# Performance work log

Measured on AMD Instinct MI355X. Metric: run time of the kernel, lower is better.

The kernel has to match this reference:

```python
import jax, jax.numpy as jnp
import numpy as np

N_NODES = 100000
HIDDEN = 128
N_EDGES = 640000


def setup_inputs() -> dict:
    key = jax.random.key(0)
    k1, k2, k3, k4 = jax.random.split(key, 4)
    z_state = jax.random.normal(k1, (N_NODES, HIDDEN), dtype=jnp.float32)
    edge_label_index = jax.random.randint(k2, (2, N_EDGES), 0, N_NODES, dtype=jnp.int64)
    # Kaiming-ish init scale for the two linear layers (torch default ~ U(-1/sqrt(fan_in), ...))
    w1 = jax.random.normal(k3, (2 * HIDDEN, HIDDEN), dtype=jnp.float32) * (1.0 / np.sqrt(2 * HIDDEN))
    b1 = jnp.zeros((HIDDEN,), dtype=jnp.float32)
    w2 = jax.random.normal(k4, (HIDDEN, 1), dtype=jnp.float32) * (1.0 / np.sqrt(HIDDEN))
    b2 = jnp.zeros((1,), dtype=jnp.float32)
    return {
        "z_state": z_state,
        "edge_label_index": edge_label_index,
        "w1": w1,
        "b1": b1,
        "w2": w2,
        "b2": b2,
    }


def reference(z_state, edge_label_index, w1, b1, w2, b2):
    # Gather source/destination node embeddings: [E, H] each.
    src = z_state[edge_label_index[0]]
    dst = z_state[edge_label_index[1]]
    # Concatenate along features -> [E, 2H], then 2-layer MLP.
    z = jnp.concatenate([src, dst], axis=-1)
    h = jax.nn.relu(z @ w1 + b1)            # [E, H]
    out = jax.nn.sigmoid(h @ w2 + b2)        # [E, 1]
    return out.reshape(-1)
```

## Files before the change

kernel.cpp:

```cpp
#include <hip/hip_runtime.h>
#include <cstdint>
#include <cstddef>

#define HD 128
#define KD 256
#define TE 128
#define BLOCK 256

typedef __attribute__((ext_vector_type(8))) short bf16x8;
typedef __attribute__((ext_vector_type(4))) float f32x4;
typedef __attribute__((ext_vector_type(4))) unsigned int u32x4;
typedef __attribute__((ext_vector_type(2))) _Float16 h16x2;

typedef const __attribute__((address_space(1))) void gv_t;
typedef __attribute__((address_space(3))) void lv_t;

__device__ __forceinline__ void gload16(const void* g, void* l) {
    __builtin_amdgcn_global_load_lds((gv_t*)g, (lv_t*)l, 16, 0, 0);
}

__device__ __forceinline__ unsigned short f2bf(float x) {
    unsigned u = __float_as_uint(x);
    u = (u + 0x7fffu + ((u >> 16) & 1u)) >> 16;
    return (unsigned short)u;
}


__global__ void pack_B_kernel(const float* __restrict__ w1,
                              unsigned short* __restrict__ Bp) {
    const int tid = blockIdx.x * 256 + threadIdx.x;
    const int lane = tid & 63, nf = (tid >> 6) & 15, kt = tid >> 10;
    const int col = nf * 16 + (lane & 15);
    const int k0 = kt * 32 + (lane >> 4) * 8;
    #pragma unroll
    for (int j = 0; j < 8; ++j) {
        const int k = k0 + j;
        const float v = (col < HD) ? w1[(size_t)k * HD + col]
                                   : w1[(size_t)(HD + k) * HD + (col - HD)];
        Bp[(size_t)tid * 8 + j] = f2bf(v);
    }
}

__global__ __launch_bounds__(256, 2) void uv_gemm_kernel(
    const float* __restrict__ z, const unsigned short* __restrict__ Bp,
    const float* __restrict__ b1, _Float16* __restrict__ UV, const int NN)
{
    __shared__ __attribute__((aligned(16))) unsigned short sA[128 * HD];
    char* sAb = (char*)sA;
    const int t = threadIdx.x, wave = t >> 6, l = t & 63;
    const int n0 = blockIdx.x * 128;
    {
        const int r = t >> 1, kh = t & 1;
        int n = n0 + r; if (n >= NN) n = NN - 1;
        const float* zr = z + (size_t)n * HD + kh * 64;
        #pragma unroll
        for (int q = 0; q < 16; ++q) {
            const float4 v = *(const float4*)(zr + q * 4);
            ushort4 o;
            o.x = f2bf(v.x); o.y = f2bf(v.y); o.z = f2bf(v.z); o.w = f2bf(v.w);
            const int byte = r * 256 + (kh * 64 + q * 4) * 2;
            *(ushort4*)(sAb + (byte ^ ((r & 15) << 4))) = o;
        }
    }
    __syncthreads();

    const int waveM = wave >> 1, waveN = wave & 1;
    f32x4 acc[4][8];
    #pragma unroll
    for (int nf = 0; nf < 8; ++nf) {
        const int c = waveN * 128 + nf * 16 + (l & 15);
        const float iv = (c < HD) ? b1[c] : 0.f;
        #pragma unroll
        for (int mf = 0; mf < 4; ++mf)
            #pragma unroll
            for (int j = 0; j < 4; ++j) acc[mf][nf][j] = iv;
    }
    #pragma unroll
    for (int kt = 0; kt < 4; ++kt) {
        bf16x8 bfr[8], af[4];
        #pragma unroll
        for (int nf = 0; nf < 8; ++nf)
            bfr[nf] = *(const bf16x8*)(Bp + (size_t)((kt * 16 + waveN * 8 + nf) * 64 + l) * 8);
        #pragma unroll
        for (int mf = 0; mf < 4; ++mf) {
            const int rr = waveM * 64 + mf * 16 + (l & 15);
            const int byte = rr * 256 + kt * 64 + (l >> 4) * 16;
            af[mf] = *(const bf16x8*)(sAb + (byte ^ ((rr & 15) << 4)));
        }
        #pragma unroll
        for (int mf = 0; mf < 4; ++mf)
            #pragma unroll
            for (int nf = 0; nf < 8; ++nf)
                acc[mf][nf] = __builtin_amdgcn_mfma_f32_16x16x32_bf16(
                    af[mf], bfr[nf], acc[mf][nf], 0, 0, 0);
    }
    #pragma unroll
    for (int mf = 0; mf < 4; ++mf)
        #pragma unroll
        for (int j = 0; j < 4; ++j) {
            const int rr = waveM * 64 + mf * 16 + (l >> 4) * 4 + j;
            const int n2 = n0 + rr;
            if (n2 < NN) {
                #pragma unroll
                for (int nf = 0; nf < 8; ++nf) {
                    const int c = waveN * 128 + nf * 16 + (l & 15);
                    UV[(size_t)n2 * KD + c] = (_Float16)acc[mf][nf][j];
                }
            }
        }
}

__global__ __launch_bounds__(256, 8) void edge_uv_f16_kernel(
    const _Float16* __restrict__ UV, const int* __restrict__ eli,
    const int E, const float* __restrict__ w2, const float* __restrict__ b2,
    float* __restrict__ out)
{
    const int t = threadIdx.x;
    const int cl = t & 15;
    const int gid = (blockIdx.x * 256 + t) >> 4;
    const int ng = (gridDim.x * 256) >> 4;

    h16x2 w2h[4];
    {
        const float4 wlo = *(const float4*)(w2 + cl * 8);
        const float4 whi = *(const float4*)(w2 + cl * 8 + 4);
        w2h[0] = (h16x2){(_Float16)wlo.x, (_Float16)wlo.y};
        w2h[1] = (h16x2){(_Float16)wlo.z, (_Float16)wlo.w};
        w2h[2] = (h16x2){(_Float16)whi.x, (_Float16)whi.y};
        w2h[3] = (h16x2){(_Float16)whi.z, (_Float16)whi.w};
    }
    const float bb2 = b2[0];
    const h16x2 zero2 = (h16x2){(_Float16)0.f, (_Float16)0.f};

    int e = gid;
    if (e >= E) return;

    int s = eli[e], d = eli[E + e];
    u32x4 u = *(const u32x4*)(UV + (size_t)s * KD + cl * 8);
    u32x4 v = *(const u32x4*)(UV + (size_t)d * KD + HD + cl * 8);
    int en = e + ng;
    int enc = (en < E) ? en : (E - 1);
    int sn = eli[enc], dn = eli[E + enc];

    for (;;) {
        const int e2 = en + ng;
        const int e2c = (e2 < E) ? e2 : (E - 1);
        const int s2 = eli[e2c], d2 = eli[E + e2c];
        const u32x4 un = *(const u32x4*)(UV + (size_t)sn * KD + cl * 8);
        const u32x4 vn = *(const u32x4*)(UV + (size_t)dn * KD + HD + cl * 8);

        h16x2 acc2 = zero2;
        #pragma unroll
        for (int m = 0; m < 4; ++m) {
            union { unsigned int ui; h16x2 h2; } cu, cv;
            cu.ui = u[m]; cv.ui = v[m];
            const h16x2 h = __builtin_elementwise_max(cu.h2 + cv.h2, zero2);
            acc2 = acc2 + h * w2h[m];
        }
        float acc = (float)acc2[0] + (float)acc2[1];
        #pragma unroll
        for (int msk = 1; msk <= 8; msk <<= 1) acc += __shfl_xor(acc, msk);
        if (cl == 0) out[e] = 1.f / (1.f + __expf(-(acc + bb2)));

        if (en >= E) break;
        e = en; u = un; v = vn;
        en = e2; sn = s2; dn = d2;
    }
}


__global__ void convert_z_kernel(const float* __restrict__ z,
                                 unsigned short* __restrict__ zb, int n4) {
    int i = blockIdx.x * blockDim.x + threadIdx.x;
    if (i < n4) {
        float4 v = ((const float4*)z)[i];
        ushort4 o;
        o.x = f2bf(v.x); o.y = f2bf(v.y); o.z = f2bf(v.z); o.w = f2bf(v.w);
        ((ushort4*)zb)[i] = o;
    }
}

__global__ void pack_w1_kernel(const float* __restrict__ w1,
                               unsigned short* __restrict__ w1p) {
    int tid = blockIdx.x * blockDim.x + threadIdx.x;
    int lane = tid & 63, nf = (tid >> 6) & 7, kt = tid >> 9;
    int col = nf * 16 + (lane & 15);
    int k0 = kt * 32 + (lane >> 4) * 8;
    #pragma unroll
    for (int j = 0; j < 8; ++j)
        w1p[(size_t)tid * 8 + j] = f2bf(w1[(size_t)(k0 + j) * HD + col]);
}

__global__ __launch_bounds__(BLOCK, 2) void edge_mfma_kernel(
    const unsigned short* __restrict__ zb, const unsigned short* __restrict__ w1p,
    const int* __restrict__ eli, const int E,
    const float* __restrict__ b1, const float* __restrict__ w2,
    const float* __restrict__ b2, float* __restrict__ out)
{
    __shared__ __attribute__((aligned(16))) unsigned short sZ[TE * KD];
    __shared__ __attribute__((aligned(16))) unsigned short sW[2][8 * 64 * 8];
    const int t = threadIdx.x, wave = t >> 6, l = t & 63;
    const int e0 = blockIdx.x * TE;
    #pragma unroll
    for (int q = 0; q < 16; ++q) {
        const int epair = wave * 32 + q * 2;
        const int r = epair + (l >> 5);
        int ge = e0 + r; if (ge >= E) ge = E - 1;
        const int ob = ((l & 31) * 16) ^ ((r & 7) << 4);
        const int node = (ob < 256) ? eli[ge] : eli[E + ge];
        gload16((const char*)zb + (size_t)node * 256 + (ob & 255), (char*)sZ + epair * 512);
    }
    #pragma unroll
    for (int q = 0; q < 2; ++q) {
        const int i = wave * 2 + q;
        gload16((const char*)w1p + i * 1024 + l * 16, (char*)sW[0] + i * 1024);
    }
    __syncthreads();
    const int waveM = wave >> 1, waveN = wave & 1;
    f32x4 acc[4][4];
    #pragma unroll
    for (int i = 0; i < 4; ++i)
        #pragma unroll
        for (int j = 0; j < 4; ++j) acc[i][j] = (f32x4)(0.f);
    for (int kt = 0; kt < 8; ++kt) {
        const int buf = kt & 1;
        if (kt < 7) {
            #pragma unroll
            for (int q = 0; q < 2; ++q) {
                const int i = wave * 2 + q;
                gload16((const char*)w1p + (size_t)(kt + 1) * 8192 + i * 1024 + l * 16,
                        (char*)sW[buf ^ 1] + i * 1024);
            }
        }
        bf16x8 af[4], bfr[4];
        #pragma unroll
        for (int mf = 0; mf < 4; ++mf) {
            const int r = waveM * 64 + mf * 16 + (l & 15);
            const int o = r * 512 + kt * 64 + ((l >> 4) * 16);
            af[mf] = *(const bf16x8*)((const char*)sZ + (o ^ ((r & 7) << 4)));
        }
        #pragma unroll
        for (int nf = 0; nf < 4; ++nf)
            bfr[nf] = *(const bf16x8*)((const char*)sW[buf] + (waveN * 4 + nf) * 1024 + l * 16);
        #pragma unroll
        for (int mf = 0; mf < 4; ++mf)
            #pragma unroll
            for (int nf = 0; nf < 4; ++nf)
                acc[mf][nf] = __builtin_amdgcn_mfma_f32_16x16x32_bf16(
                    af[mf], bfr[nf], acc[mf][nf], 0, 0, 0);
        __syncthreads();
    }
    float b1v[4], w2v[4];
    #pragma unroll
    for (int nf = 0; nf < 4; ++nf) {
        const int c = waveN * 64 + nf * 16 + (l & 15);
        b1v[nf] = b1[c]; w2v[nf] = w2[c];
    }
    float part[4][4];
    #pragma unroll
    for (int mf = 0; mf < 4; ++mf)
        #pragma unroll
        for (int j = 0; j < 4; ++j) {
            float p = 0.f;
            #pragma unroll
            for (int nf = 0; nf < 4; ++nf)
                p += fmaxf(acc[mf][nf][j] + b1v[nf], 0.f) * w2v[nf];
            #pragma unroll
            for (int m = 1; m <= 8; m <<= 1) p += __shfl_xor(p, m);
            part[mf][j] = p;
        }
    float* sRed = (float*)sW;
    if (waveN == 1 && (l & 15) == 0) {
        #pragma unroll
        for (int mf = 0; mf < 4; ++mf)
            #pragma unroll
            for (int j = 0; j < 4; ++j)
                sRed[waveM * 64 + mf * 16 + (l >> 4) * 4 + j] = part[mf][j];
    }
    __syncthreads();
    if (waveN == 0 && (l & 15) == 0) {
        const float bb2 = b2[0];
        #pragma unroll
        for (int mf = 0; mf < 4; ++mf)
            #pragma unroll
            for (int j = 0; j < 4; ++j) {
                const int row = waveM * 64 + mf * 16 + (l >> 4) * 4 + j;
                const int ge = e0 + row;
                if (ge < E) out[ge] = 1.f / (1.f + __expf(-(part[mf][j] + sRed[row] + bb2)));
            }
    }
}


__global__ __launch_bounds__(256, 2) void edge_decoder_fp32_kernel(
    const float* __restrict__ z, const int* __restrict__ eli, const int E,
    const float* __restrict__ w1, const float* __restrict__ b1,
    const float* __restrict__ w2, const float* __restrict__ b2,
    float* __restrict__ out)
{
    __shared__ float sZ[32][256];
    __shared__ float sW[2][32][128];
    const int t = threadIdx.x, wave = t >> 6, lane = t & 63;
    const int e0 = blockIdx.x * 32;
    #pragma unroll
    for (int q = 0; q < 8; ++q) {
        const int e = wave * 8 + q;
        int ge = e0 + e; if (ge >= E) ge = E - 1;
        const int node = (lane < 32) ? eli[ge] : eli[E + ge];
        gload16(z + (size_t)node * HD + (size_t)(lane & 31) * 4, &sZ[e][0]);
    }
    #pragma unroll
    for (int q = 0; q < 4; ++q) {
        const int inst = wave * 4 + q;
        gload16(w1 + inst * 256 + lane * 4, &sW[0][0][0] + inst * 256);
    }
    __syncthreads();
    const int cg = t & 31, eg = t >> 5, c0 = cg * 4;
    float acc[4][4] = {{0.f,0.f,0.f,0.f}};
    for (int kc = 0; kc < 8; ++kc) {
        const int buf = kc & 1;
        if (kc + 1 < 8) {
            const float* gw = w1 + (size_t)(kc + 1) * 32 * HD;
            #pragma unroll
            for (int q = 0; q < 4; ++q) {
                const int inst = wave * 4 + q;
                gload16(gw + inst * 256 + lane * 4, &sW[buf ^ 1][0][0] + inst * 256);
            }
        }
        #pragma unroll
        for (int k4 = 0; k4 < 8; ++k4) {
            float zr[4][4];
            #pragma unroll
            for (int i = 0; i < 4; ++i)
                *(float4*)(&zr[i][0]) = *(const float4*)(&sZ[eg*4+i][kc*32 + k4*4]);
            #pragma unroll
            for (int kk = 0; kk < 4; ++kk) {
                const float4 wv = *(const float4*)(&sW[buf][k4*4+kk][c0]);
                #pragma unroll
                for (int i = 0; i < 4; ++i) {
                    acc[i][0] = fmaf(zr[i][kk], wv.x, acc[i][0]);
                    acc[i][1] = fmaf(zr[i][kk], wv.y, acc[i][1]);
                    acc[i][2] = fmaf(zr[i][kk], wv.z, acc[i][2]);
                    acc[i][3] = fmaf(zr[i][kk], wv.w, acc[i][3]);
                }
            }
        }
        __syncthreads();
    }
    const float4 b1v = *(const float4*)(&b1[c0]);
    const float4 w2v = *(const float4*)(&w2[c0]);
    const float bb2 = b2[0];
    float part[4];
    #pragma unroll
    for (int i = 0; i < 4; ++i)
        part[i] = fmaxf(acc[i][0]+b1v.x,0.f)*w2v.x + fmaxf(acc[i][1]+b1v.y,0.f)*w2v.y
                + fmaxf(acc[i][2]+b1v.z,0.f)*w2v.z + fmaxf(acc[i][3]+b1v.w,0.f)*w2v.w;
    #pragma unroll
    for (int m = 16; m >= 1; m >>= 1)
        #pragma unroll
        for (int i = 0; i < 4; ++i) part[i] += __shfl_xor(part[i], m, 32);
    if (cg == 0) {
        #pragma unroll
        for (int i = 0; i < 4; ++i) {
            const int ge = e0 + eg * 4 + i;
            if (ge < E) out[ge] = 1.0f / (1.0f + __expf(-(part[i] + bb2)));
        }
    }
}

extern "C" void kernel_launch(void* const* d_in, const int* in_sizes, int n_in,
                              void* d_out, int out_size, void* d_ws, size_t ws_size,
                              hipStream_t stream) {
    const float* z  = (const float*)d_in[0];
    const int* eli  = (const int*)d_in[1];
    const float* w1 = (const float*)d_in[2];
    const float* b1 = (const float*)d_in[3];
    const float* w2 = (const float*)d_in[4];
    const float* b2 = (const float*)d_in[5];
    float* out = (float*)d_out;

    const int E  = in_sizes[1] / 2;
    const int NN = in_sizes[0] / HD;

    const size_t uv_bytes = (size_t)NN * KD * 2;
    const size_t need_new = uv_bytes + 65536;
    const size_t need_mid = 65536 + (size_t)NN * HD * 2;

    if (ws_size >= need_new) {
        _Float16* UV = (_Float16*)d_ws;
        unsigned short* Bp = (unsigned short*)((char*)d_ws + uv_bytes);
        pack_B_kernel<<<16, 256, 0, stream>>>(w1, Bp);
        uv_gemm_kernel<<<(NN + 127) / 128, 256, 0, stream>>>(z, Bp, b1, UV, NN);
        edge_uv_f16_kernel<<<2048, 256, 0, stream>>>(UV, eli, E, w2, b2, out);
    } else if (ws_size >= need_mid) {
        unsigned short* w1p = (unsigned short*)d_ws;
        unsigned short* zb  = (unsigned short*)((char*)d_ws + 65536);
        const int n4 = NN * HD / 4;
        convert_z_kernel<<<(n4 + 255) / 256, 256, 0, stream>>>(z, zb, n4);
        pack_w1_kernel<<<16, 256, 0, stream>>>(w1, w1p);
        edge_mfma_kernel<<<(E + TE - 1) / TE, BLOCK, 0, stream>>>(
            zb, w1p, eli, E, b1, w2, b2, out);
    } else {
        edge_decoder_fp32_kernel<<<(E + 31) / 32, 256, 0, stream>>>(
            z, eli, E, w1, b1, w2, b2, out);
    }
}
```

Before: 84.41 us.

## Bucket edges by source node and assign buckets per XCD for UV gather locality

```diff
diff --git a/kernel.cpp b/kernel.cpp
--- a/kernel.cpp
+++ b/kernel.cpp
@@ -4,13 +4,13 @@
 
 #define HD 128
 #define KD 256
-#define TE 128
-#define BLOCK 256
+#define NBMAX 512
 
 typedef __attribute__((ext_vector_type(8))) short bf16x8;
 typedef __attribute__((ext_vector_type(4))) float f32x4;
 typedef __attribute__((ext_vector_type(4))) unsigned int u32x4;
 typedef __attribute__((ext_vector_type(2))) _Float16 h16x2;
+typedef __attribute__((ext_vector_type(4))) _Float16 h16x4;
 
 typedef const __attribute__((address_space(1))) void gv_t;
 typedef __attribute__((address_space(3))) void lv_t;
@@ -68,12 +68,13 @@
     f32x4 acc[4][8];
     #pragma unroll
     for (int nf = 0; nf < 8; ++nf) {
-        const int c = waveN * 128 + nf * 16 + (l & 15);
-        const float iv = (c < HD) ? b1[c] : 0.f;
-        #pragma unroll
-        for (int mf = 0; mf < 4; ++mf)
-            #pragma unroll
-            for (int j = 0; j < 4; ++j) acc[mf][nf][j] = iv;
+        float4 bv = make_float4(0.f, 0.f, 0.f, 0.f);
+        if (waveN == 0) bv = *(const float4*)(b1 + nf * 16 + (l >> 4) * 4);
+        #pragma unroll
+        for (int mf = 0; mf < 4; ++mf) {
+            acc[mf][nf][0] = bv.x; acc[mf][nf][1] = bv.y;
+            acc[mf][nf][2] = bv.z; acc[mf][nf][3] = bv.w;
+        }
     }
     #pragma unroll
     for (int kt = 0; kt < 4; ++kt) {
@@ -92,23 +93,150 @@
             #pragma unroll
             for (int nf = 0; nf < 8; ++nf)
                 acc[mf][nf] = __builtin_amdgcn_mfma_f32_16x16x32_bf16(
-                    af[mf], bfr[nf], acc[mf][nf], 0, 0, 0);
-    }
-    #pragma unroll
-    for (int mf = 0; mf < 4; ++mf)
-        #pragma unroll
-        for (int j = 0; j < 4; ++j) {
-            const int rr = waveM * 64 + mf * 16 + (l >> 4) * 4 + j;
-            const int n2 = n0 + rr;
-            if (n2 < NN) {
-                #pragma unroll
-                for (int nf = 0; nf < 8; ++nf) {
-                    const int c = waveN * 128 + nf * 16 + (l & 15);
-                    UV[(size_t)n2 * KD + c] = (_Float16)acc[mf][nf][j];
-                }
+                    bfr[nf], af[mf], acc[mf][nf], 0, 0, 0);
+    }
+    #pragma unroll
+    for (int mf = 0; mf < 4; ++mf) {
+        const int n2 = n0 + waveM * 64 + mf * 16 + (l & 15);
+        if (n2 < NN) {
+            #pragma unroll
+            for (int nf = 0; nf < 8; ++nf) {
+                const int c0 = waveN * 128 + nf * 16 + (l >> 4) * 4;
+                h16x4 o = (h16x4){(_Float16)acc[mf][nf][0], (_Float16)acc[mf][nf][1],
+                                  (_Float16)acc[mf][nf][2], (_Float16)acc[mf][nf][3]};
+                *(h16x4*)(UV + (size_t)n2 * KD + c0) = o;
             }
         }
-}
+    }
+}
+
+
+__global__ void hist_kernel(const int* __restrict__ eli, const int E,
+                            const int nb, int* __restrict__ hist) {
+    __shared__ int lh[NBMAX];
+    const int t = threadIdx.x;
+    for (int b = t; b < nb; b += 256) lh[b] = 0;
+    __syncthreads();
+    const int per = (E + gridDim.x - 1) / gridDim.x;
+    const int e0 = blockIdx.x * per;
+    int e1 = e0 + per; if (e1 > E) e1 = E;
+    for (int e = e0 + t; e < e1; e += 256)
+        atomicAdd(&lh[eli[e] >> 8], 1);
+    __syncthreads();
+    for (int b = t; b < nb; b += 256)
+        if (lh[b]) atomicAdd(&hist[b], lh[b]);
+}
+
+__global__ void scan_kernel(const int* __restrict__ hist, const int nb,
+                            int* __restrict__ start, int* __restrict__ cursor) {
+    __shared__ int sc[NBMAX];
+    const int t = threadIdx.x;
+    const int own = (t < nb) ? hist[t] : 0;
+    sc[t] = own;
+    __syncthreads();
+    for (int off = 1; off < NBMAX; off <<= 1) {
+        const int v = (t >= off) ? sc[t - off] : 0;
+        __syncthreads();
+        sc[t] += v;
+        __syncthreads();
+    }
+    if (t < nb) {
+        const int ex = sc[t] - own;
+        start[t] = ex; cursor[t] = ex;
+    }
+    if (t == nb - 1) start[nb] = sc[t];
+}
+
+__global__ void scatter_kernel(const int* __restrict__ eli, const int E,
+                               const int nb, int* __restrict__ cursor,
+                               int* __restrict__ sorted) {
+    __shared__ int lh[NBMAX];
+    __shared__ int lb[NBMAX];
+    const int t = threadIdx.x;
+    for (int b = t; b < nb; b += 256) lh[b] = 0;
+    __syncthreads();
+    const int per = (E + gridDim.x - 1) / gridDim.x;
+    const int e0 = blockIdx.x * per;
+    int e1 = e0 + per; if (e1 > E) e1 = E;
+    for (int e = e0 + t; e < e1; e += 256)
+        atomicAdd(&lh[eli[e] >> 8], 1);
+    __syncthreads();
+    for (int b = t; b < nb; b += 256) {
+        const int c = lh[b];
+        lb[b] = c ? atomicAdd(&cursor[b], c) : 0;
+        lh[b] = 0;
+    }
+    __syncthreads();
+    for (int e = e0 + t; e < e1; e += 256) {
+        const int s = eli[e];
+        const int r = atomicAdd(&lh[s >> 8], 1);
+        int* p = sorted + (size_t)(lb[s >> 8] + r) * 3;
+        p[0] = s; p[1] = eli[E + e]; p[2] = e;
+    }
+}
+
+
+__global__ __launch_bounds__(256, 8) void edge_sorted_kernel(
+    const _Float16* __restrict__ UV, const int* __restrict__ sorted,
+    const int* __restrict__ start, const int NB,
+    const float* __restrict__ w2, const float* __restrict__ b2,
+    float* __restrict__ out)
+{
+    const int t = threadIdx.x, cl = t & 15, g = t >> 4;
+    const int xcd = blockIdx.x & 7, rank = blockIdx.x >> 3;
+    const int nbx = gridDim.x >> 3;
+    const int bpx = (NB + 7) >> 3;
+    const int blo = xcd * bpx;
+    if (blo >= NB) return;
+    int bhi = blo + bpx; if (bhi > NB) bhi = NB;
+    const int elo = start[blo], ehi = start[bhi];
+
+    h16x2 w2h[4];
+    {
+        const float4 wlo = *(const float4*)(w2 + cl * 8);
+        const float4 whi = *(const float4*)(w2 + cl * 8 + 4);
+        w2h[0] = (h16x2){(_Float16)wlo.x, (_Float16)wlo.y};
+        w2h[1] = (h16x2){(_Float16)wlo.z, (_Float16)wlo.w};
+        w2h[2] = (h16x2){(_Float16)whi.x, (_Float16)whi.y};
+        w2h[3] = (h16x2){(_Float16)whi.z, (_Float16)whi.w};
+    }
+    const float bb2 = b2[0];
+    const h16x2 zero2 = (h16x2){(_Float16)0.f, (_Float16)0.f};
+
+    const int stride = nbx * 16;
+    int i = elo + rank * 16 + g;
+    if (i >= ehi) return;
+    const int* tp = sorted + (size_t)i * 3;
+    int e = tp[2];
+    u32x4 u = *(const u32x4*)(UV + (size_t)tp[0] * KD + cl * 8);
+    u32x4 v = *(const u32x4*)(UV + (size_t)tp[1] * KD + HD + cl * 8);
+
+    for (;;) {
+        const int i2 = i + stride;
+        int e2 = 0; u32x4 un, vn;
+        if (i2 < ehi) {
+            const int* tq = sorted + (size_t)i2 * 3;
+            e2 = tq[2];
+            un = *(const u32x4*)(UV + (size_t)tq[0] * KD + cl * 8);
+            vn = *(const u32x4*)(UV + (size_t)tq[1] * KD + HD + cl * 8);
+        }
+        h16x2 acc2 = zero2;
+        #pragma unroll
+        for (int m = 0; m < 4; ++m) {
+            union { unsigned int ui; h16x2 h2; } cu, cv;
+            cu.ui = u[m]; cv.ui = v[m];
+            const h16x2 h = __builtin_elementwise_max(cu.h2 + cv.h2, zero2);
+            acc2 = acc2 + h * w2h[m];
+        }
+        float acc = (float)acc2[0] + (float)acc2[1];
+        #pragma unroll
+        for (int msk = 1; msk <= 8; msk <<= 1) acc += __shfl_xor(acc, msk);
+        if (cl == 0) out[e] = 1.f / (1.f + __expf(-(acc + bb2)));
+        if (i2 >= ehi) break;
+        i = i2; e = e2; u = un; v = vn;
+    }
+}
+
 
 __global__ __launch_bounds__(256, 8) void edge_uv_f16_kernel(
     const _Float16* __restrict__ UV, const int* __restrict__ eli,
@@ -134,7 +262,6 @@
 
     int e = gid;
     if (e >= E) return;
-
     int s = eli[e], d = eli[E + e];
     u32x4 u = *(const u32x4*)(UV + (size_t)s * KD + cl * 8);
     u32x4 v = *(const u32x4*)(UV + (size_t)d * KD + HD + cl * 8);
@@ -165,129 +292,6 @@
         if (en >= E) break;
         e = en; u = un; v = vn;
         en = e2; sn = s2; dn = d2;
-    }
-}
-
-
-__global__ void convert_z_kernel(const float* __restrict__ z,
-                                 unsigned short* __restrict__ zb, int n4) {
-    int i = blockIdx.x * blockDim.x + threadIdx.x;
-    if (i < n4) {
-        float4 v = ((const float4*)z)[i];
-        ushort4 o;
-        o.x = f2bf(v.x); o.y = f2bf(v.y); o.z = f2bf(v.z); o.w = f2bf(v.w);
-        ((ushort4*)zb)[i] = o;
-    }
-}
-
-__global__ void pack_w1_kernel(const float* __restrict__ w1,
-                               unsigned short* __restrict__ w1p) {
-    int tid = blockIdx.x * blockDim.x + threadIdx.x;
-    int lane = tid & 63, nf = (tid >> 6) & 7, kt = tid >> 9;
-    int col = nf * 16 + (lane & 15);
-    int k0 = kt * 32 + (lane >> 4) * 8;
-    #pragma unroll
-    for (int j = 0; j < 8; ++j)
-        w1p[(size_t)tid * 8 + j] = f2bf(w1[(size_t)(k0 + j) * HD + col]);
-}
-
-__global__ __launch_bounds__(BLOCK, 2) void edge_mfma_kernel(
-    const unsigned short* __restrict__ zb, const unsigned short* __restrict__ w1p,
-    const int* __restrict__ eli, const int E,
-    const float* __restrict__ b1, const float* __restrict__ w2,
-    const float* __restrict__ b2, float* __restrict__ out)
-{
-    __shared__ __attribute__((aligned(16))) unsigned short sZ[TE * KD];
-    __shared__ __attribute__((aligned(16))) unsigned short sW[2][8 * 64 * 8];
-    const int t = threadIdx.x, wave = t >> 6, l = t & 63;
-    const int e0 = blockIdx.x * TE;
-    #pragma unroll
-    for (int q = 0; q < 16; ++q) {
-        const int epair = wave * 32 + q * 2;
-        const int r = epair + (l >> 5);
-        int ge = e0 + r; if (ge >= E) ge = E - 1;
-        const int ob = ((l & 31) * 16) ^ ((r & 7) << 4);
-        const int node = (ob < 256) ? eli[ge] : eli[E + ge];
-        gload16((const char*)zb + (size_t)node * 256 + (ob & 255), (char*)sZ + epair * 512);
-    }
-    #pragma unroll
-    for (int q = 0; q < 2; ++q) {
-        const int i = wave * 2 + q;
-        gload16((const char*)w1p + i * 1024 + l * 16, (char*)sW[0] + i * 1024);
-    }
-    __syncthreads();
-    const int waveM = wave >> 1, waveN = wave & 1;
-    f32x4 acc[4][4];
-    #pragma unroll
-    for (int i = 0; i < 4; ++i)
-        #pragma unroll
-        for (int j = 0; j < 4; ++j) acc[i][j] = (f32x4)(0.f);
-    for (int kt = 0; kt < 8; ++kt) {
-        const int buf = kt & 1;
-        if (kt < 7) {
-            #pragma unroll
-            for (int q = 0; q < 2; ++q) {
-                const int i = wave * 2 + q;
-                gload16((const char*)w1p + (size_t)(kt + 1) * 8192 + i * 1024 + l * 16,
-                        (char*)sW[buf ^ 1] + i * 1024);
-            }
-        }
-        bf16x8 af[4], bfr[4];
-        #pragma unroll
-        for (int mf = 0; mf < 4; ++mf) {
-            const int r = waveM * 64 + mf * 16 + (l & 15);
-            const int o = r * 512 + kt * 64 + ((l >> 4) * 16);
-            af[mf] = *(const bf16x8*)((const char*)sZ + (o ^ ((r & 7) << 4)));
-        }
-        #pragma unroll
-        for (int nf = 0; nf < 4; ++nf)
-            bfr[nf] = *(const bf16x8*)((const char*)sW[buf] + (waveN * 4 + nf) * 1024 + l * 16);
-        #pragma unroll
-        for (int mf = 0; mf < 4; ++mf)
-            #pragma unroll
-            for (int nf = 0; nf < 4; ++nf)
-                acc[mf][nf] = __builtin_amdgcn_mfma_f32_16x16x32_bf16(
-                    af[mf], bfr[nf], acc[mf][nf], 0, 0, 0);
-        __syncthreads();
-    }
-    float b1v[4], w2v[4];
-    #pragma unroll
-    for (int nf = 0; nf < 4; ++nf) {
-        const int c = waveN * 64 + nf * 16 + (l & 15);
-        b1v[nf] = b1[c]; w2v[nf] = w2[c];
-    }
-    float part[4][4];
-    #pragma unroll
-    for (int mf = 0; mf < 4; ++mf)
-        #pragma unroll
-        for (int j = 0; j < 4; ++j) {
-            float p = 0.f;
-            #pragma unroll
-            for (int nf = 0; nf < 4; ++nf)
-                p += fmaxf(acc[mf][nf][j] + b1v[nf], 0.f) * w2v[nf];
-            #pragma unroll
-            for (int m = 1; m <= 8; m <<= 1) p += __shfl_xor(p, m);
-            part[mf][j] = p;
-        }
-    float* sRed = (float*)sW;
-    if (waveN == 1 && (l & 15) == 0) {
-        #pragma unroll
-        for (int mf = 0; mf < 4; ++mf)
-            #pragma unroll
-            for (int j = 0; j < 4; ++j)
-                sRed[waveM * 64 + mf * 16 + (l >> 4) * 4 + j] = part[mf][j];
-    }
-    __syncthreads();
-    if (waveN == 0 && (l & 15) == 0) {
-        const float bb2 = b2[0];
-        #pragma unroll
-        for (int mf = 0; mf < 4; ++mf)
-            #pragma unroll
-            for (int j = 0; j < 4; ++j) {
-                const int row = waveM * 64 + mf * 16 + (l >> 4) * 4 + j;
-                const int ge = e0 + row;
-                if (ge < E) out[ge] = 1.f / (1.f + __expf(-(part[mf][j] + sRed[row] + bb2)));
-            }
     }
 }
 
@@ -381,25 +385,40 @@
 
     const int E  = in_sizes[1] / 2;
     const int NN = in_sizes[0] / HD;
-
-    const size_t uv_bytes = (size_t)NN * KD * 2;
-    const size_t need_new = uv_bytes + 65536;
-    const size_t need_mid = 65536 + (size_t)NN * HD * 2;
-
-    if (ws_size >= need_new) {
-        _Float16* UV = (_Float16*)d_ws;
-        unsigned short* Bp = (unsigned short*)((char*)d_ws + uv_bytes);
+    const int NB = (NN + 255) >> 8;
+
+    size_t off = 0;
+    auto take = [&](size_t n) { size_t r = off; off = (off + n + 15) & ~(size_t)15; return r; };
+    const size_t o_uv    = take((size_t)NN * KD * 2);
+    const size_t o_bp    = take(65536);
+    const size_t need_uv = off;
+    const size_t o_hist  = take(NBMAX * 4);
+    const size_t o_start = take((NBMAX + 1) * 4);
+    const size_t o_cur   = take(NBMAX * 4);
+    const size_t o_sort  = take((size_t)E * 12);
+    const size_t need_sorted = off;
+
+    if (ws_size >= need_sorted && NB <= NBMAX) {
+        _Float16* UV = (_Float16*)((char*)d_ws + o_uv);
+        unsigned short* Bp = (unsigned short*)((char*)d_ws + o_bp);
+        int* hist   = (int*)((char*)d_ws + o_hist);
+        int* start  = (int*)((char*)d_ws + o_start);
+        int* cursor = (int*)((char*)d_ws + o_cur);
+        int* sorted = (int*)((char*)d_ws + o_sort);
+
+        hipMemsetAsync(hist, 0, NBMAX * 4, stream);
+        pack_B_kernel<<<16, 256, 0, stream>>>(w1, Bp);
+        hist_kernel<<<256, 256, 0, stream>>>(eli, E, NB, hist);
+        scan_kernel<<<1, NBMAX, 0, stream>>>(hist, NB, start, cursor);
+        scatter_kernel<<<256, 256, 0, stream>>>(eli, E, NB, cursor, sorted);
+        uv_gemm_kernel<<<(NN + 127) / 128, 256, 0, stream>>>(z, Bp, b1, UV, NN);
+        edge_sorted_kernel<<<2048, 256, 0, stream>>>(UV, sorted, start, NB, w2, b2, out);
+    } else if (ws_size >= need_uv) {
+        _Float16* UV = (_Float16*)((char*)d_ws + o_uv);
+        unsigned short* Bp = (unsigned short*)((char*)d_ws + o_bp);
         pack_B_kernel<<<16, 256, 0, stream>>>(w1, Bp);
         uv_gemm_kernel<<<(NN + 127) / 128, 256, 0, stream>>>(z, Bp, b1, UV, NN);
         edge_uv_f16_kernel<<<2048, 256, 0, stream>>>(UV, eli, E, w2, b2, out);
-    } else if (ws_size >= need_mid) {
-        unsigned short* w1p = (unsigned short*)d_ws;
-        unsigned short* zb  = (unsigned short*)((char*)d_ws + 65536);
-        const int n4 = NN * HD / 4;
-        convert_z_kernel<<<(n4 + 255) / 256, 256, 0, stream>>>(z, zb, n4);
-        pack_w1_kernel<<<16, 256, 0, stream>>>(w1, w1p);
-        edge_mfma_kernel<<<(E + TE - 1) / TE, BLOCK, 0, stream>>>(
-            zb, w1p, eli, E, b1, w2, b2, out);
     } else {
         edge_decoder_fp32_kernel<<<(E + 31) / 32, 256, 0, stream>>>(
             z, eli, E, w1, b1, w2, b2, out);
```

New measurement: 110.2 us. 1.31x slower.
